# Kernel tuning notes

Hardware: AMD Instinct MI355X
Metric: run time of the kernel (lower is better)

Reference implementation:

```python
import jax, jax.numpy as jnp
import numpy as np

VOCAB, E, H = 32000, 256, 256
B, T = 64, 2048


def setup_inputs() -> dict:
    key = jax.random.key(0)
    ks = jax.random.split(key, 6)
    X = jax.random.randint(ks[0], (B, T), 0, VOCAB)
    emb = jax.random.normal(ks[1], (VOCAB, E), dtype=jnp.float32)
    W_qrnn = jax.random.normal(ks[2], (E, 3 * H), dtype=jnp.float32) / np.sqrt(E)
    b_qrnn = jnp.zeros((3 * H,), dtype=jnp.float32)
    c0 = jax.random.normal(ks[3], (B, H), dtype=jnp.float32)
    W_out = jax.random.normal(ks[4], (H, 1), dtype=jnp.float32) / np.sqrt(H)
    b_out = jnp.zeros((1,), dtype=jnp.float32)
    return {"X": X, "emb": emb, "W_qrnn": W_qrnn, "b_qrnn": b_qrnn,
            "c0": c0, "W_out": W_out, "b_out": b_out}


def reference(X, emb, W_qrnn, b_qrnn, c0, W_out, b_out):
    # Embedding lookup: [B,T] -> [B,T,E]; permute to seq-major [T,B,E]
    x = jnp.transpose(emb[X], (1, 0, 2))
    # QRNN window=1 gate projection: all timesteps in one GEMM, [T,B,3H]
    g = jnp.einsum('tbe,ef->tbf', x, W_qrnn) + b_qrnn
    z, f, o = jnp.split(g, 3, axis=-1)
    z = jnp.tanh(z)
    f = jax.nn.sigmoid(f)
    o = jax.nn.sigmoid(o)

    # fo-pooling recurrence: c_t = f_t * c_{t-1} + (1 - f_t) * z_t
    def step(c, zf):
        z_t, f_t = zf
        c = f_t * c + (1.0 - f_t) * z_t
        return c, c

    _, cs = jax.lax.scan(step, c0, (z, f))  # cs: [T,B,H]
    h = o * cs                              # h_t = o_t * c_t
    hn = h[-1]                              # last timestep, [B,H]
    return hn @ W_out + b_out               # [B,1]
```

## Files before the change

kernel.cpp:

```cpp
#include <hip/hip_runtime.h>
#include <hip/hip_bf16.h>
#include <math.h>

#define EDIM 256
#define HDIM 256
#define BDIM 64
#define TDIM 2048
#define NC   64
#define TC   32
#define CPB  4

typedef __attribute__((ext_vector_type(8)))  short  short8;
typedef __attribute__((ext_vector_type(4)))  float  floatx4;
typedef __attribute__((ext_vector_type(4)))  unsigned int uintx4;

__device__ __forceinline__ unsigned short f2bf(float f) {
    unsigned int u = __float_as_uint(f);
    u += 0x7FFFu + ((u >> 16) & 1u);
    return (unsigned short)(u >> 16);
}
__device__ __forceinline__ unsigned int pk2(float a, float b) {
    return (unsigned int)f2bf(a) | ((unsigned int)f2bf(b) << 16);
}
__device__ __forceinline__ float sigm(float x) {
    return __builtin_amdgcn_rcpf(1.f + __expf(-x));
}
__device__ __forceinline__ float tanh_fast(float x) {
    return fmaf(-2.f, __builtin_amdgcn_rcpf(1.f + __expf(2.f * x)), 1.f);
}

__global__ __launch_bounds__(256) void qrnn_pack(
    const float* __restrict__ Wq, const float* __restrict__ emb,
    unsigned short* __restrict__ Wp, unsigned short* __restrict__ ebf)
{
    const int bx = blockIdx.x;
    if (bx < 256) {
        const int nt = (bx >> 3) & 7;
        const int hg = bx >> 6;
        const int ks = bx & 7;
        const int t = threadIdx.x;
        const int lane = t >> 2, pj = t & 3;
        const int col = lane & 15, q = lane >> 4;
        const int h = hg * 64 + (nt & 3) * 16 + col;
        const int c = (nt < 4) ? h : (HDIM + h);
        const int k = ks * 32 + q * 8 + pj * 2;
        unsigned int v = pk2(Wq[k * (3 * HDIM) + c], Wq[(k + 1) * (3 * HDIM) + c]);
        *(unsigned int*)(Wp + (size_t)bx * 512 + lane * 8 + pj * 2) = v;
    } else {
        size_t i = ((size_t)(bx - 256) * 256 + threadIdx.x) * 8;
        floatx4 a = *(const floatx4*)(emb + i);
        floatx4 b = *(const floatx4*)(emb + i + 4);
        uintx4 o = {pk2(a.x, a.y), pk2(a.z, a.w), pk2(b.x, b.y), pk2(b.z, b.w)};
        *(uintx4*)(ebf + i) = o;
    }
}

template<bool EMBBF>
__global__ __launch_bounds__(256, 2) void qrnn_mfma(
    const int* __restrict__ X, const float* __restrict__ emb,
    const unsigned short* __restrict__ ebf, const unsigned short* __restrict__ Wp,
    const float* __restrict__ bq, float* __restrict__ wsA, float* __restrict__ wsB)
{
    __shared__ __align__(16) short Bsh[32768];

    const int tid = threadIdx.x;
    const int cg = blockIdx.x, bg = blockIdx.y, hg = blockIdx.z;
    const int lane = tid & 63, w = tid >> 6;
    const int col = lane & 15, q = lane >> 4;

    const unsigned short* wpb = Wp + (size_t)hg * 32768;
#pragma unroll
    for (int i = 0; i < 16; ++i) {
        const int ch = w * 16 + i;
        __builtin_amdgcn_global_load_lds(
            (const __attribute__((address_space(1))) unsigned int*)(wpb + ch * 512 + lane * 8),
            (__attribute__((address_space(3))) unsigned int*)(Bsh + ch * 512),
            16, 0, 0);
    }

    const int b0 = bg * 8 + 2 * w;
    int xid[CPB][4];
#pragma unroll
    for (int c = 0; c < CPB; ++c)
#pragma unroll
        for (int mt = 0; mt < 4; ++mt)
            xid[c][mt] = X[(b0 + (mt >> 1)) * TDIM + (cg * CPB + c) * TC + (mt & 1) * 16 + col];

    const int hbase = hg * 64;
    float bz[4], bff[4];
#pragma unroll
    for (int nt = 0; nt < 4; ++nt) {
        bz[nt]  = bq[hbase + nt * 16 + col];
        bff[nt] = bq[HDIM + hbase + nt * 16 + col];
    }

    short8 abuf[3][4];
    auto fetchA = [&](int c, int ks, int slot) {
#pragma unroll
        for (int mt = 0; mt < 4; ++mt) {
            if constexpr (EMBBF) {
                abuf[slot][mt] = *(const short8*)(ebf + (size_t)xid[c][mt] * EDIM + q * 8 + ks * 32);
            } else {
                const float* ap = emb + (size_t)xid[c][mt] * EDIM + q * 8 + ks * 32;
                floatx4 f0 = *(const floatx4*)ap;
                floatx4 f1 = *(const floatx4*)(ap + 4);
                uintx4 p = {pk2(f0.x, f0.y), pk2(f0.z, f0.w),
                            pk2(f1.x, f1.y), pk2(f1.z, f1.w)};
                abuf[slot][mt] = *(short8*)&p;
            }
        }
    };

    floatx4 acc[4][8];
#pragma unroll
    for (int mt = 0; mt < 4; ++mt)
#pragma unroll
        for (int nt = 0; nt < 8; ++nt) acc[mt][nt] = (floatx4){0.f, 0.f, 0.f, 0.f};

    fetchA(0, 0, 0);
    fetchA(0, 1, 1);
    __syncthreads();

#pragma unroll
    for (int c = 0; c < CPB; ++c) {
#pragma unroll
        for (int ks = 0; ks < 8; ++ks) {
            const int s = c * 8 + ks;
            if (s + 2 < CPB * 8)
                fetchA((s + 2) >> 3, (s + 2) & 7, (s + 2) % 3);
            short8 bf[8];
#pragma unroll
            for (int nt = 0; nt < 8; ++nt)
                bf[nt] = *(const short8*)(Bsh + (nt * 8 + ks) * 512 + lane * 8);
            const int sl = s % 3;
#pragma unroll
            for (int nt = 0; nt < 8; ++nt)
#pragma unroll
                for (int mt = 0; mt < 4; ++mt)
                    acc[mt][nt] = __builtin_amdgcn_mfma_f32_16x16x32_bf16(abuf[sl][mt], bf[nt], acc[mt][nt], 0, 0, 0);
        }

        const int cc = cg * CPB + c;
        float Af0[4], Bf0[4], Af1[4], Bf1[4];
#pragma unroll
        for (int nt = 0; nt < 4; ++nt) {
            float Aseg[4], Bseg[4];
#pragma unroll
            for (int mt = 0; mt < 4; ++mt) {
                float Ac = 1.f, Bc = 0.f;
#pragma unroll
                for (int j = 0; j < 4; ++j) {
                    float z = tanh_fast(acc[mt][nt][j] + bz[nt]);
                    float f = sigm(acc[mt][nt + 4][j] + bff[nt]);
                    Ac = f * Ac;
                    Bc = fmaf(f, Bc, (1.f - f) * z);
                }
                Aseg[mt] = Ac; Bseg[mt] = Bc;
            }
#pragma unroll
            for (int st = 0; st < 2; ++st) {
                const int msk = 16 << st;
                const bool self_earlier = ((q >> st) & 1) == 0;
#pragma unroll
                for (int mt = 0; mt < 4; ++mt) {
                    float Ap = __shfl_xor(Aseg[mt], msk, 64);
                    float Bp = __shfl_xor(Bseg[mt], msk, 64);
                    Bseg[mt] = self_earlier ? fmaf(Ap, Bseg[mt], Bp)
                                            : fmaf(Aseg[mt], Bp, Bseg[mt]);
                    Aseg[mt] = Aseg[mt] * Ap;
                }
            }
            Af0[nt] = Aseg[0] * Aseg[1];
            Bf0[nt] = fmaf(Aseg[1], Bseg[0], Bseg[1]);
            Af1[nt] = Aseg[2] * Aseg[3];
            Bf1[nt] = fmaf(Aseg[3], Bseg[2], Bseg[3]);
        }

        float As0 = (q == 0) ? Af0[0] : (q == 1) ? Af0[1] : (q == 2) ? Af0[2] : Af0[3];
        float Bs0 = (q == 0) ? Bf0[0] : (q == 1) ? Bf0[1] : (q == 2) ? Bf0[2] : Bf0[3];
        float As1 = (q == 0) ? Af1[0] : (q == 1) ? Af1[1] : (q == 2) ? Af1[2] : Af1[3];
        float Bs1 = (q == 0) ? Bf1[0] : (q == 1) ? Bf1[1] : (q == 2) ? Bf1[2] : Bf1[3];

        const size_t r0 = ((size_t)cc * BDIM + b0) * HDIM + hbase + lane;
        wsA[r0] = As0;          wsB[r0] = Bs0;
        wsA[r0 + HDIM] = As1;   wsB[r0 + HDIM] = Bs1;

#pragma unroll
        for (int mt = 0; mt < 4; ++mt)
#pragma unroll
            for (int nt = 0; nt < 8; ++nt) acc[mt][nt] = (floatx4){0.f, 0.f, 0.f, 0.f};
    }
}

__global__ __launch_bounds__(256) void qrnn_combine(
    const float* __restrict__ wsA, const float* __restrict__ wsB,
    const float* __restrict__ c0, const int* __restrict__ X,
    const float* __restrict__ emb, const float* __restrict__ Wq,
    const float* __restrict__ bq, const float* __restrict__ Wout,
    const float* __restrict__ bout, float* __restrict__ out)
{
    const int b = blockIdx.x;
    const int h = threadIdx.x;

    float c = c0[b * HDIM + h];
    for (int c8 = 0; c8 < NC; c8 += 8) {
        float a[8], bb[8];
#pragma unroll
        for (int i = 0; i < 8; ++i) {
            size_t base = ((size_t)(c8 + i) * BDIM + b) * HDIM + h;
            a[i]  = wsA[base];
            bb[i] = wsB[base];
        }
#pragma unroll
        for (int i = 0; i < 8; ++i) c = fmaf(a[i], c, bb[i]);
    }

    __shared__ float xs[EDIM];
    int idx = X[b * TDIM + (TDIM - 1)];
    xs[h] = emb[(size_t)idx * EDIM + h];
    __syncthreads();

    float acc = 0.f;
#pragma unroll 16
    for (int e = 0; e < EDIM; ++e)
        acc = fmaf(xs[e], Wq[e * (3 * HDIM) + 2 * HDIM + h], acc);

    float o  = 1.f / (1.f + expf(-(acc + bq[2 * HDIM + h])));
    float hn = o * c;

    __shared__ float red[HDIM];
    red[h] = hn * Wout[h];
    __syncthreads();
    for (int s = HDIM / 2; s > 0; s >>= 1) {
        if (h < s) red[h] += red[h + s];
        __syncthreads();
    }
    if (h == 0) out[b] = red[0] + bout[0];
}

extern "C" void kernel_launch(void* const* d_in, const int* in_sizes, int n_in,
                              void* d_out, int out_size, void* d_ws, size_t ws_size,
                              hipStream_t stream) {
    const int*   X    = (const int*)d_in[0];
    const float* emb  = (const float*)d_in[1];
    const float* Wq   = (const float*)d_in[2];
    const float* bq   = (const float*)d_in[3];
    const float* c0   = (const float*)d_in[4];
    const float* Wout = (const float*)d_in[5];
    const float* bout = (const float*)d_in[6];
    float* out = (float*)d_out;

    float* wsA = (float*)d_ws;
    float* wsB = wsA + (size_t)NC * BDIM * HDIM;
    unsigned short* Wp  = (unsigned short*)(wsB + (size_t)NC * BDIM * HDIM);
    unsigned short* ebf = Wp + (size_t)256 * 512;

    const size_t need_full = (size_t)2 * NC * BDIM * HDIM * 4
                           + (size_t)256 * 512 * 2
                           + (size_t)32000 * EDIM * 2;
    const bool full = ws_size >= need_full;

    const int emb_blocks = (32000 * EDIM / 8) / 256;
    qrnn_pack<<<256 + (full ? emb_blocks : 0), 256, 0, stream>>>(Wq, emb, Wp, ebf);

    dim3 g(NC / CPB, BDIM / 8, HDIM / 64);
    if (full) qrnn_mfma<true ><<<g, 256, 0, stream>>>(X, emb, ebf, Wp, bq, wsA, wsB);
    else      qrnn_mfma<false><<<g, 256, 0, stream>>>(X, emb, ebf, Wp, bq, wsA, wsB);

    qrnn_combine<<<BDIM, 256, 0, stream>>>(wsA, wsB, c0, X, emb, Wq, bq, Wout, bout, out);
}
```

Measured before the change: 150.3 us.

## Pre-gather embeddings into MFMA-ready bf16 tiles per batch chunk

Adds a mode in which the pack kernel gathers the embedding rows for every token, converts them to bf16 and stores them in the exact per-lane fragment layout the MFMA kernel reads. The MFMA kernel then does contiguous coalesced 16-byte loads instead of random row gathers indexed by token ids. This replaces converting the whole 32000-row table with gathering only the B*T rows actually used. The cost is a larger workspace (B*T*E*2 bytes), and the new path runs only when the workspace is large enough.

```diff
diff --git a/kernel.cpp b/kernel.cpp
--- a/kernel.cpp
+++ b/kernel.cpp
@@ -31,7 +31,9 @@
 
 __global__ __launch_bounds__(256) void qrnn_pack(
     const float* __restrict__ Wq, const float* __restrict__ emb,
-    unsigned short* __restrict__ Wp, unsigned short* __restrict__ ebf)
+    const int* __restrict__ X,
+    unsigned short* __restrict__ Wp, unsigned short* __restrict__ aux,
+    int mode)
 {
     const int bx = blockIdx.x;
     if (bx < 256) {
@@ -46,19 +48,39 @@
         const int k = ks * 32 + q * 8 + pj * 2;
         unsigned int v = pk2(Wq[k * (3 * HDIM) + c], Wq[(k + 1) * (3 * HDIM) + c]);
         *(unsigned int*)(Wp + (size_t)bx * 512 + lane * 8 + pj * 2) = v;
+    } else if (mode == 2) {
+        const int bx2 = bx - 256;
+        const int b = bx2 >> 6, cc = bx2 & 63;
+        __shared__ int tok[TC];
+        if (threadIdx.x < TC)
+            tok[threadIdx.x] = X[b * TDIM + cc * TC + threadIdx.x];
+        __syncthreads();
+        unsigned short* xb = aux + (size_t)bx2 * 8192;
+#pragma unroll
+        for (int r = 0; r < 4; ++r) {
+            const int ci = r * 256 + threadIdx.x;
+            const int col = ci & 15, q = (ci >> 4) & 3;
+            const int th = (ci >> 6) & 1, ks = ci >> 7;
+            const int t = th * 16 + col;
+            const float* src = emb + (size_t)tok[t] * EDIM + ks * 32 + q * 8;
+            floatx4 a = *(const floatx4*)src;
+            floatx4 c4 = *(const floatx4*)(src + 4);
+            uintx4 o = {pk2(a.x, a.y), pk2(a.z, a.w), pk2(c4.x, c4.y), pk2(c4.z, c4.w)};
+            *(uintx4*)(xb + (size_t)ci * 8) = o;
+        }
     } else {
         size_t i = ((size_t)(bx - 256) * 256 + threadIdx.x) * 8;
         floatx4 a = *(const floatx4*)(emb + i);
         floatx4 b = *(const floatx4*)(emb + i + 4);
         uintx4 o = {pk2(a.x, a.y), pk2(a.z, a.w), pk2(b.x, b.y), pk2(b.z, b.w)};
-        *(uintx4*)(ebf + i) = o;
-    }
-}
-
-template<bool EMBBF>
+        *(uintx4*)(aux + i) = o;
+    }
+}
+
+template<int MODE>
 __global__ __launch_bounds__(256, 2) void qrnn_mfma(
     const int* __restrict__ X, const float* __restrict__ emb,
-    const unsigned short* __restrict__ ebf, const unsigned short* __restrict__ Wp,
+    const unsigned short* __restrict__ aux, const unsigned short* __restrict__ Wp,
     const float* __restrict__ bq, float* __restrict__ wsA, float* __restrict__ wsB)
 {
     __shared__ __align__(16) short Bsh[32768];
@@ -80,11 +102,13 @@
 
     const int b0 = bg * 8 + 2 * w;
     int xid[CPB][4];
-#pragma unroll
-    for (int c = 0; c < CPB; ++c)
-#pragma unroll
-        for (int mt = 0; mt < 4; ++mt)
-            xid[c][mt] = X[(b0 + (mt >> 1)) * TDIM + (cg * CPB + c) * TC + (mt & 1) * 16 + col];
+    if constexpr (MODE < 2) {
+#pragma unroll
+        for (int c = 0; c < CPB; ++c)
+#pragma unroll
+            for (int mt = 0; mt < 4; ++mt)
+                xid[c][mt] = X[(b0 + (mt >> 1)) * TDIM + (cg * CPB + c) * TC + (mt & 1) * 16 + col];
+    }
 
     const int hbase = hg * 64;
     float bz[4], bff[4];
@@ -98,8 +122,11 @@
     auto fetchA = [&](int c, int ks, int slot) {
 #pragma unroll
         for (int mt = 0; mt < 4; ++mt) {
-            if constexpr (EMBBF) {
-                abuf[slot][mt] = *(const short8*)(ebf + (size_t)xid[c][mt] * EDIM + q * 8 + ks * 32);
+            if constexpr (MODE == 2) {
+                const size_t bb = (size_t)(b0 + (mt >> 1)) * NC + (cg * CPB + c);
+                abuf[slot][mt] = *(const short8*)(aux + ((bb * 8 + ks) * 2 + (mt & 1)) * 512 + lane * 8);
+            } else if constexpr (MODE == 1) {
+                abuf[slot][mt] = *(const short8*)(aux + (size_t)xid[c][mt] * EDIM + q * 8 + ks * 32);
             } else {
                 const float* ap = emb + (size_t)xid[c][mt] * EDIM + q * 8 + ks * 32;
                 floatx4 f0 = *(const floatx4*)ap;
@@ -253,19 +280,23 @@
     float* wsA = (float*)d_ws;
     float* wsB = wsA + (size_t)NC * BDIM * HDIM;
     unsigned short* Wp  = (unsigned short*)(wsB + (size_t)NC * BDIM * HDIM);
-    unsigned short* ebf = Wp + (size_t)256 * 512;
-
-    const size_t need_full = (size_t)2 * NC * BDIM * HDIM * 4
-                           + (size_t)256 * 512 * 2
-                           + (size_t)32000 * EDIM * 2;
-    const bool full = ws_size >= need_full;
-
-    const int emb_blocks = (32000 * EDIM / 8) / 256;
-    qrnn_pack<<<256 + (full ? emb_blocks : 0), 256, 0, stream>>>(Wq, emb, Wp, ebf);
+    unsigned short* aux = Wp + (size_t)256 * 512;
+
+    const size_t wsAB = (size_t)2 * NC * BDIM * HDIM * 4;
+    const size_t wpsz = (size_t)256 * 512 * 2;
+    const size_t need2 = wsAB + wpsz + (size_t)BDIM * TDIM * EDIM * 2;
+    const size_t need1 = wsAB + wpsz + (size_t)32000 * EDIM * 2;
+    const int mode = (ws_size >= need2) ? 2 : (ws_size >= need1 ? 1 : 0);
+
+    const int gather_blocks = (mode == 2) ? (BDIM * NC)
+                            : (mode == 1) ? (32000 * EDIM / 8) / 256
+                            : 0;
+    qrnn_pack<<<256 + gather_blocks, 256, 0, stream>>>(Wq, emb, X, Wp, aux, mode);
 
     dim3 g(NC / CPB, BDIM / 8, HDIM / 64);
-    if (full) qrnn_mfma<true ><<<g, 256, 0, stream>>>(X, emb, ebf, Wp, bq, wsA, wsB);
-    else      qrnn_mfma<false><<<g, 256, 0, stream>>>(X, emb, ebf, Wp, bq, wsA, wsB);
+    if      (mode == 2) qrnn_mfma<2><<<g, 256, 0, stream>>>(X, emb, aux, Wp, bq, wsA, wsB);
+    else if (mode == 1) qrnn_mfma<1><<<g, 256, 0, stream>>>(X, emb, aux, Wp, bq, wsA, wsB);
+    else                qrnn_mfma<0><<<g, 256, 0, stream>>>(X, emb, aux, Wp, bq, wsA, wsB);
 
     qrnn_combine<<<BDIM, 256, 0, stream>>>(wsA, wsB, c0, X, emb, Wq, bq, Wout, bout, out);
 }
```

New measurement: 171.5 us. 14.2% more time.

## Fuse pack, MFMA and combine kernels into one persistent kernel with grid barriers

Applied to the files above, without the earlier changes.

Merges the three launches (weight/embedding bf16 pack, MFMA chunk scan, final combine) into a single kernel. Each block packs its own W slice straight into LDS and converts a strided share of the embedding table, then all blocks meet at an atomic-counter grid barrier before the GEMM. A second counter barrier lets the first 64 blocks run the combine step. This removes launch gaps and the Wp global round trip. In exchange it relies on all 512 blocks being co-resident for the spin barriers, adds a memset, and every block now re-reads and re-converts the W slice from fp32.

```diff
diff --git a/kernel.cpp b/kernel.cpp
--- a/kernel.cpp
+++ b/kernel.cpp
@@ -2,6 +2,7 @@
 #include <hip/hip_bf16.h>
 #include <math.h>
 
+#define VOCAB 32000
 #define EDIM 256
 #define HDIM 256
 #define BDIM 64
@@ -9,6 +10,7 @@
 #define NC   64
 #define TC   32
 #define CPB  4
+#define NBLK 512
 
 typedef __attribute__((ext_vector_type(8)))  short  short8;
 typedef __attribute__((ext_vector_type(4)))  float  floatx4;
@@ -29,53 +31,46 @@
     return fmaf(-2.f, __builtin_amdgcn_rcpf(1.f + __expf(2.f * x)), 1.f);
 }
 
-__global__ __launch_bounds__(256) void qrnn_pack(
-    const float* __restrict__ Wq, const float* __restrict__ emb,
-    unsigned short* __restrict__ Wp, unsigned short* __restrict__ ebf)
-{
-    const int bx = blockIdx.x;
-    if (bx < 256) {
-        const int nt = (bx >> 3) & 7;
-        const int hg = bx >> 6;
-        const int ks = bx & 7;
-        const int t = threadIdx.x;
-        const int lane = t >> 2, pj = t & 3;
-        const int col = lane & 15, q = lane >> 4;
-        const int h = hg * 64 + (nt & 3) * 16 + col;
-        const int c = (nt < 4) ? h : (HDIM + h);
-        const int k = ks * 32 + q * 8 + pj * 2;
-        unsigned int v = pk2(Wq[k * (3 * HDIM) + c], Wq[(k + 1) * (3 * HDIM) + c]);
-        *(unsigned int*)(Wp + (size_t)bx * 512 + lane * 8 + pj * 2) = v;
-    } else {
-        size_t i = ((size_t)(bx - 256) * 256 + threadIdx.x) * 8;
-        floatx4 a = *(const floatx4*)(emb + i);
-        floatx4 b = *(const floatx4*)(emb + i + 4);
-        uintx4 o = {pk2(a.x, a.y), pk2(a.z, a.w), pk2(b.x, b.y), pk2(b.z, b.w)};
-        *(uintx4*)(ebf + i) = o;
-    }
-}
-
-template<bool EMBBF>
-__global__ __launch_bounds__(256, 2) void qrnn_mfma(
+template<int MODE>
+__global__ __launch_bounds__(256, 2) void qrnn_fused(
     const int* __restrict__ X, const float* __restrict__ emb,
-    const unsigned short* __restrict__ ebf, const unsigned short* __restrict__ Wp,
-    const float* __restrict__ bq, float* __restrict__ wsA, float* __restrict__ wsB)
+    const float* __restrict__ Wq, const float* __restrict__ bq,
+    const float* __restrict__ c0, const float* __restrict__ Wout,
+    const float* __restrict__ bout,
+    unsigned short* __restrict__ ebf, float* __restrict__ wsA,
+    float* __restrict__ wsB, unsigned int* __restrict__ cnt,
+    float* __restrict__ out)
 {
     __shared__ __align__(16) short Bsh[32768];
 
     const int tid = threadIdx.x;
     const int cg = blockIdx.x, bg = blockIdx.y, hg = blockIdx.z;
+    const int fid = cg + 16 * bg + 128 * hg;
     const int lane = tid & 63, w = tid >> 6;
     const int col = lane & 15, q = lane >> 4;
 
-    const unsigned short* wpb = Wp + (size_t)hg * 32768;
-#pragma unroll
-    for (int i = 0; i < 16; ++i) {
-        const int ch = w * 16 + i;
-        __builtin_amdgcn_global_load_lds(
-            (const __attribute__((address_space(1))) unsigned int*)(wpb + ch * 512 + lane * 8),
-            (__attribute__((address_space(3))) unsigned int*)(Bsh + ch * 512),
-            16, 0, 0);
+    {
+        const int l2 = tid >> 2, pj = tid & 3;
+        const int dcol = l2 & 15, dq = l2 >> 4;
+#pragma unroll 4
+        for (int ch = 0; ch < 64; ++ch) {
+            const int nt = ch >> 3, ks = ch & 7;
+            const int h = hg * 64 + (nt & 3) * 16 + dcol;
+            const int c = (nt < 4) ? h : (HDIM + h);
+            const int k = ks * 32 + dq * 8 + pj * 2;
+            unsigned int v = pk2(Wq[k * (3 * HDIM) + c], Wq[(k + 1) * (3 * HDIM) + c]);
+            *(unsigned int*)(Bsh + ch * 512 + l2 * 8 + pj * 2) = v;
+        }
+    }
+
+    if constexpr (MODE == 1) {
+        for (int g = fid * 256 + tid; g < (VOCAB * EDIM / 8); g += NBLK * 256) {
+            const float* src = emb + (size_t)g * 8;
+            floatx4 a = *(const floatx4*)src;
+            floatx4 b = *(const floatx4*)(src + 4);
+            uintx4 o = {pk2(a.x, a.y), pk2(a.z, a.w), pk2(b.x, b.y), pk2(b.z, b.w)};
+            *(uintx4*)(ebf + (size_t)g * 8) = o;
+        }
     }
 
     const int b0 = bg * 8 + 2 * w;
@@ -94,11 +89,25 @@
         bff[nt] = bq[HDIM + hbase + nt * 16 + col];
     }
 
+    __syncthreads();
+    if constexpr (MODE == 1) {
+        if (tid == 0) {
+            __hip_atomic_fetch_add(&cnt[0], 1u, __ATOMIC_ACQ_REL, __HIP_MEMORY_SCOPE_AGENT);
+            unsigned int v;
+            do {
+                __builtin_amdgcn_s_sleep(32);
+                v = __hip_atomic_load(&cnt[0], __ATOMIC_RELAXED, __HIP_MEMORY_SCOPE_AGENT);
+            } while (v < NBLK);
+        }
+        __syncthreads();
+        __builtin_amdgcn_fence(__ATOMIC_ACQUIRE, "agent");
+    }
+
     short8 abuf[3][4];
     auto fetchA = [&](int c, int ks, int slot) {
 #pragma unroll
         for (int mt = 0; mt < 4; ++mt) {
-            if constexpr (EMBBF) {
+            if constexpr (MODE == 1) {
                 abuf[slot][mt] = *(const short8*)(ebf + (size_t)xid[c][mt] * EDIM + q * 8 + ks * 32);
             } else {
                 const float* ap = emb + (size_t)xid[c][mt] * EDIM + q * 8 + ks * 32;
@@ -119,7 +128,6 @@
 
     fetchA(0, 0, 0);
     fetchA(0, 1, 1);
-    __syncthreads();
 
 #pragma unroll
     for (int c = 0; c < CPB; ++c) {
@@ -190,52 +198,60 @@
 #pragma unroll
             for (int nt = 0; nt < 8; ++nt) acc[mt][nt] = (floatx4){0.f, 0.f, 0.f, 0.f};
     }
-}
-
-__global__ __launch_bounds__(256) void qrnn_combine(
-    const float* __restrict__ wsA, const float* __restrict__ wsB,
-    const float* __restrict__ c0, const int* __restrict__ X,
-    const float* __restrict__ emb, const float* __restrict__ Wq,
-    const float* __restrict__ bq, const float* __restrict__ Wout,
-    const float* __restrict__ bout, float* __restrict__ out)
-{
-    const int b = blockIdx.x;
-    const int h = threadIdx.x;
-
-    float c = c0[b * HDIM + h];
-    for (int c8 = 0; c8 < NC; c8 += 8) {
-        float a[8], bb[8];
-#pragma unroll
-        for (int i = 0; i < 8; ++i) {
-            size_t base = ((size_t)(c8 + i) * BDIM + b) * HDIM + h;
-            a[i]  = wsA[base];
-            bb[i] = wsB[base];
-        }
-#pragma unroll
-        for (int i = 0; i < 8; ++i) c = fmaf(a[i], c, bb[i]);
-    }
-
-    __shared__ float xs[EDIM];
-    int idx = X[b * TDIM + (TDIM - 1)];
-    xs[h] = emb[(size_t)idx * EDIM + h];
+
     __syncthreads();
-
-    float acc = 0.f;
+    if (tid == 0)
+        __hip_atomic_fetch_add(&cnt[1], 1u, __ATOMIC_ACQ_REL, __HIP_MEMORY_SCOPE_AGENT);
+    if (fid >= BDIM) return;
+    if (tid == 0) {
+        unsigned int v;
+        do {
+            __builtin_amdgcn_s_sleep(32);
+            v = __hip_atomic_load(&cnt[1], __ATOMIC_RELAXED, __HIP_MEMORY_SCOPE_AGENT);
+        } while (v < NBLK);
+    }
+    __syncthreads();
+    __builtin_amdgcn_fence(__ATOMIC_ACQUIRE, "agent");
+
+    {
+        const int b = fid;
+        const int h = tid;
+
+        float cacc = c0[b * HDIM + h];
+        for (int c8 = 0; c8 < NC; c8 += 8) {
+            float a[8], bb[8];
+#pragma unroll
+            for (int i = 0; i < 8; ++i) {
+                size_t base = ((size_t)(c8 + i) * BDIM + b) * HDIM + h;
+                a[i]  = wsA[base];
+                bb[i] = wsB[base];
+            }
+#pragma unroll
+            for (int i = 0; i < 8; ++i) cacc = fmaf(a[i], cacc, bb[i]);
+        }
+
+        float* xs = (float*)Bsh;
+        float* red = (float*)Bsh + EDIM;
+        int idx = X[b * TDIM + (TDIM - 1)];
+        xs[h] = emb[(size_t)idx * EDIM + h];
+        __syncthreads();
+
+        float dacc = 0.f;
 #pragma unroll 16
-    for (int e = 0; e < EDIM; ++e)
-        acc = fmaf(xs[e], Wq[e * (3 * HDIM) + 2 * HDIM + h], acc);
-
-    float o  = 1.f / (1.f + expf(-(acc + bq[2 * HDIM + h])));
-    float hn = o * c;
-
-    __shared__ float red[HDIM];
-    red[h] = hn * Wout[h];
-    __syncthreads();
-    for (int s = HDIM / 2; s > 0; s >>= 1) {
-        if (h < s) red[h] += red[h + s];
+        for (int e = 0; e < EDIM; ++e)
+            dacc = fmaf(xs[e], Wq[e * (3 * HDIM) + 2 * HDIM + h], dacc);
+
+        float o  = 1.f / (1.f + expf(-(dacc + bq[2 * HDIM + h])));
+        float hn = o * cacc;
+
+        red[h] = hn * Wout[h];
         __syncthreads();
-    }
-    if (h == 0) out[b] = red[0] + bout[0];
+        for (int s = HDIM / 2; s > 0; s >>= 1) {
+            if (h < s) red[h] += red[h + s];
+            __syncthreads();
+        }
+        if (h == 0) out[b] = red[0] + bout[0];
+    }
 }
 
 extern "C" void kernel_launch(void* const* d_in, const int* in_sizes, int n_in,
@@ -250,22 +266,22 @@
     const float* bout = (const float*)d_in[6];
     float* out = (float*)d_out;
 
-    float* wsA = (float*)d_ws;
+    unsigned int* cnt = (unsigned int*)d_ws;
+    float* wsA = (float*)((char*)d_ws + 256);
     float* wsB = wsA + (size_t)NC * BDIM * HDIM;
-    unsigned short* Wp  = (unsigned short*)(wsB + (size_t)NC * BDIM * HDIM);
-    unsigned short* ebf = Wp + (size_t)256 * 512;
-
-    const size_t need_full = (size_t)2 * NC * BDIM * HDIM * 4
-                           + (size_t)256 * 512 * 2
-                           + (size_t)32000 * EDIM * 2;
-    const bool full = ws_size >= need_full;
-
-    const int emb_blocks = (32000 * EDIM / 8) / 256;
-    qrnn_pack<<<256 + (full ? emb_blocks : 0), 256, 0, stream>>>(Wq, emb, Wp, ebf);
+    unsigned short* ebf = (unsigned short*)(wsB + (size_t)NC * BDIM * HDIM);
+
+    const size_t wsAB  = (size_t)2 * NC * BDIM * HDIM * 4;
+    const size_t need1 = 256 + wsAB + (size_t)VOCAB * EDIM * 2;
+    const int mode = (ws_size >= need1) ? 1 : 0;
+
+    (void)hipMemsetAsync(cnt, 0, 16, stream);
 
     dim3 g(NC / CPB, BDIM / 8, HDIM / 64);
-    if (full) qrnn_mfma<true ><<<g, 256, 0, stream>>>(X, emb, ebf, Wp, bq, wsA, wsB);
-    else      qrnn_mfma<false><<<g, 256, 0, stream>>>(X, emb, ebf, Wp, bq, wsA, wsB);
-
-    qrnn_combine<<<BDIM, 256, 0, stream>>>(wsA, wsB, c0, X, emb, Wq, bq, Wout, bout, out);
-}
+    if (mode == 1)
+        qrnn_fused<1><<<g, 256, 0, stream>>>(X, emb, Wq, bq, c0, Wout, bout,
+                                             ebf, wsA, wsB, cnt, out);
+    else
+        qrnn_fused<0><<<g, 256, 0, stream>>>(X, emb, Wq, bq, c0, Wout, bout,
+                                             ebf, wsA, wsB, cnt, out);
+}
```

Result: slower. 226.7 us (+50.9%).
